# Performance work log

Hardware: AMD Instinct MI355X
Metric: run time of the kernel (lower is better)

The kernel has to match this reference:

```python
import jax, jax.numpy as jnp
import numpy as np

N_ATOMS = 100000
N_EDGES = 3200000
N_RBF = 8
HIDDEN = 16
NUM_GRAPHS = 1


def setup_inputs() -> dict:
    key = jax.random.key(0)
    ks = jax.random.split(key, 10)
    positions = jax.random.normal(ks[0], (N_ATOMS, 3), dtype=jnp.float32)
    vectors = jax.random.normal(ks[1], (N_EDGES, 3), dtype=jnp.float32)
    local_or_ghost = jax.random.uniform(ks[2], (N_ATOMS,), dtype=jnp.float32)
    W1 = jax.random.normal(ks[3], (N_RBF, HIDDEN), dtype=jnp.float32) * 0.1
    b1 = jax.random.normal(ks[4], (HIDDEN,), dtype=jnp.float32) * 0.1
    W2 = jax.random.normal(ks[5], (HIDDEN, HIDDEN), dtype=jnp.float32) * 0.1
    w3 = jax.random.normal(ks[6], (HIDDEN,), dtype=jnp.float32) * 0.1
    field = jax.random.normal(ks[7], (3,), dtype=jnp.float32) * 0.01
    alphas = jax.random.uniform(ks[8], (N_RBF,), dtype=jnp.float32, minval=0.1, maxval=1.1)
    edge_index = jax.random.randint(ks[9], (2, N_EDGES), 0, N_ATOMS, dtype=jnp.int64)
    batch = jnp.zeros((N_ATOMS,), dtype=jnp.int64)
    return {"positions": positions, "vectors": vectors, "local_or_ghost": local_or_ghost,
            "W1": W1, "b1": b1, "W2": W2, "w3": w3, "field": field, "alphas": alphas,
            "edge_index": edge_index, "batch": batch}


def _node_energy(positions, vectors, W1, b1, W2, w3, field, alphas, receiver, n_atoms):
    # Surrogate MACE-like energy: radial basis on edge vectors -> edge MLP ->
    # scatter to receiving atom -> node MLP, plus a linear position term.
    r2 = jnp.sum(vectors * vectors, axis=-1)              # (E,)
    phi = jnp.exp(-r2[:, None] * alphas[None, :])         # (E, F)
    msg = jax.nn.silu(phi @ W1 + b1)                      # (E, H)
    h = jax.ops.segment_sum(msg, receiver, num_segments=n_atoms)  # (N, H)
    node_e = jax.nn.silu(h @ W2) @ w3 + positions @ field          # (N,)
    return node_e


def reference(positions, vectors, local_or_ghost, W1, b1, W2, w3, field, alphas, edge_index, batch):
    n_atoms = positions.shape[0]
    sender, receiver = edge_index[0], edge_index[1]

    def total_local(pos, vec):
        ne = _node_energy(pos, vec, W1, b1, W2, w3, field, alphas, receiver, n_atoms)
        return jnp.sum(ne * local_or_ghost), ne

    # forces = -dE/dpositions, edge_forces = -dE/dvectors (vectors as independent leaf)
    (_, node_energy), grads = jax.value_and_grad(total_local, argnums=(0, 1), has_aux=True)(positions, vectors)
    forces = -grads[0]
    edge_forces = -grads[1]

    node_energy_local = node_energy * local_or_ghost
    total_energy_local = jax.ops.segment_sum(node_energy_local, batch, num_segments=NUM_GRAPHS)

    # edge virial: einsum('zi,zj->zij')
    edge_virial = edge_forces[:, :, None] * vectors[:, None, :]   # (E, 3, 3)
    av_send = jax.ops.segment_sum(edge_virial, sender, num_segments=n_atoms)
    av_recv = jax.ops.segment_sum(edge_virial, receiver, num_segments=n_atoms)
    atom_virial = (av_send + av_recv) * 0.5
    atom_virial = (atom_virial + jnp.swapaxes(atom_virial, -1, -2)) * 0.5
    atom_virial = -atom_virial
    virials = jnp.sum(atom_virial, axis=0)                        # (3, 3)

    return total_energy_local, node_energy, forces, virials, atom_virial
```

## Files before the change

kernel.cpp:

```cpp
#include <hip/hip_runtime.h>

#define N_ATOMS 100000
#define N_EDGES 3200000
#define N_RBF 8
#define HIDDEN 16

#define NB 4096
#define TSCALE 64.0f

#define OFF_TE   0
#define OFF_NE   1
#define OFF_F    (1 + N_ATOMS)
#define OFF_VIR  (1 + N_ATOMS + 3*N_ATOMS)
#define OFF_AV   (OFF_VIR + 9)

#define WPAD (N_ATOMS + 4)
#define NBLK16 (N_ATOMS / 16)
#define SCAN_B 1024
#define SCAN_NB ((N_ATOMS + SCAN_B) / SCAN_B)

#define NTAB_S   0
#define NTAB_G   (NB*HIDDEN)
#define NOFF_R   (2*NB*HIDDEN)
#define NOFF_S   (NOFF_R + WPAD)
#define NCNT_R8  (NOFF_S + WPAD)
#define NCNT_S8  (NCNT_R8 + 8*WPAD)
#define NTEP     (NCNT_S8 + 8*WPAD)
#define NVPART   (NTEP + 8192)
#define NAV6R    (NVPART + 40960)
#define NPAY_R   (NAV6R + 6*N_ATOMS)
#define NDR2V    (NPAY_R + 4*N_EDGES)
#define NBSUM    NPAY_R
#define NEND     (NDR2V + 4*N_EDGES)

#define WOFF_OFFS_R 0
#define WOFF_OFFS_S WPAD
#define WOFF_RANK_R (2*WPAD)
#define WOFF_RANK_S (WOFF_RANK_R + N_EDGES)
#define WOFF_EID_R  (WOFF_RANK_S + N_EDGES)
#define WOFF_EID_S  (WOFF_EID_R + N_EDGES)
#define WOFF_DR2    (WOFF_EID_S + N_EDGES)
#define WOFF_AV6    (WOFF_DR2 + N_EDGES)
#define WOFF_END    (WOFF_AV6 + 6*N_ATOMS)

typedef float fvec4 __attribute__((ext_vector_type(4)));

__device__ inline void nt_store4(float a, float b, float c, float d, float4* p) {
    fvec4 t;
    t.x = a; t.y = b; t.z = c; t.w = d;
    __builtin_nontemporal_store(t, (fvec4*)p);
}

__device__ inline unsigned int get_xcd() {
    unsigned int xcd;
    asm volatile("s_getreg_b32 %0, hwreg(HW_REG_XCC_ID)" : "=s"(xcd));
    return xcd & 7;
}

__global__ void build_tables(const float* __restrict__ W1, const float* __restrict__ b1,
                             const float* __restrict__ alphas,
                             float* __restrict__ s_tab, float* __restrict__ g_tab) {
    int idx = blockIdx.x * blockDim.x + threadIdx.x;
    int b = idx >> 4, j = idx & 15;
    float r2 = (float)b / TSCALE;
    float pre = b1[j], pw = 0.f;
    #pragma unroll
    for (int f = 0; f < N_RBF; ++f) {
        float al = alphas[f];
        float ph = __expf(-r2 * al);
        float w  = W1[f*HIDDEN + j];
        pre += ph * w;
        pw  += al * ph * w;
    }
    float sig = 1.f / (1.f + __expf(-pre));
    s_tab[idx] = pre * sig;
    g_tab[idx] = sig * (1.f + pre * (1.f - sig)) * pw;
}


__global__ void count8_kernel(const int* __restrict__ ei,
                              int* __restrict__ cnt_r8, int* __restrict__ cnt_s8) {
    unsigned int xcd = get_xcd();
    int e = blockIdx.x * blockDim.x + threadIdx.x;
    if (e >= N_EDGES) return;
    int send = ei[e], recv = ei[N_EDGES + e];
    __hip_atomic_fetch_add(&cnt_r8[xcd * WPAD + recv], 1,
                           __ATOMIC_RELAXED, __HIP_MEMORY_SCOPE_WORKGROUP);
    __hip_atomic_fetch_add(&cnt_s8[xcd * WPAD + send], 1,
                           __ATOMIC_RELAXED, __HIP_MEMORY_SCOPE_WORKGROUP);
}

__global__ void xcd_prefix_kernel(int* __restrict__ cnt_r8, int* __restrict__ cnt_s8,
                                  int* __restrict__ offs_r, int* __restrict__ offs_s) {
    int a = blockIdx.x * blockDim.x + threadIdx.x;
    if (a >= N_ATOMS) return;
    int t = 0;
    #pragma unroll
    for (int x = 0; x < 8; ++x) {
        int c = cnt_r8[x*WPAD + a];
        cnt_r8[x*WPAD + a] = t;
        t += c;
    }
    offs_r[a] = t;
    t = 0;
    #pragma unroll
    for (int x = 0; x < 8; ++x) {
        int c = cnt_s8[x*WPAD + a];
        cnt_s8[x*WPAD + a] = t;
        t += c;
    }
    offs_s[a] = t;
}


__global__ void scanA(int* __restrict__ offs_r, int* __restrict__ offs_s,
                      int* __restrict__ bsum) {
    int y = blockIdx.y;
    int* a = y ? offs_s : offs_r;
    const int n = N_ATOMS + 1;
    int i = blockIdx.x * SCAN_B + threadIdx.x;
    int v = (i < n) ? a[i] : 0;
    int lane = threadIdx.x & 63, w = threadIdx.x >> 6;
    int s = v;
    #pragma unroll
    for (int o = 1; o < 64; o <<= 1) {
        int t = __shfl_up(s, o);
        if (lane >= o) s += t;
    }
    __shared__ int wsum[16];
    if (lane == 63) wsum[w] = s;
    __syncthreads();
    if (threadIdx.x < 16) {
        int sc = wsum[threadIdx.x];
        #pragma unroll
        for (int o = 1; o < 16; o <<= 1) {
            int t = __shfl_up(sc, o);
            if ((int)threadIdx.x >= o) sc += t;
        }
        wsum[threadIdx.x] = sc;
    }
    __syncthreads();
    int wpre = (w > 0) ? wsum[w-1] : 0;
    if (i < n) a[i] = s - v + wpre;
    if (threadIdx.x == 0) bsum[y * SCAN_NB + blockIdx.x] = wsum[15];
}

__global__ void scanB(int* __restrict__ bsum) {
    __shared__ int lds[SCAN_NB];
    for (int y = 0; y < 2; ++y) {
        if (threadIdx.x < SCAN_NB) lds[threadIdx.x] = bsum[y*SCAN_NB + threadIdx.x];
        __syncthreads();
        if (threadIdx.x == 0) {
            int run = 0;
            for (int i = 0; i < SCAN_NB; ++i) { int t = lds[i]; lds[i] = run; run += t; }
        }
        __syncthreads();
        if (threadIdx.x < SCAN_NB) bsum[y*SCAN_NB + threadIdx.x] = lds[threadIdx.x];
        __syncthreads();
    }
}

__global__ void scanC(int* __restrict__ offs_r, int* __restrict__ offs_s,
                      const int* __restrict__ bsum) {
    int y = blockIdx.y;
    int* a = y ? offs_s : offs_r;
    int i = blockIdx.x * SCAN_B + threadIdx.x;
    if (i < N_ATOMS + 1) a[i] += bsum[y*SCAN_NB + blockIdx.x];
}

__global__ void scatter1(const int* __restrict__ ei,
                         const int* __restrict__ offs_r, const int* __restrict__ offs_s,
                         int* __restrict__ cnt_r8, int* __restrict__ cnt_s8,
                         const float* __restrict__ vectors,
                         float4* __restrict__ pay_r) {
    unsigned int xcd = get_xcd();
    int e = blockIdx.x * blockDim.x + threadIdx.x;
    if (e >= N_EDGES) return;
    int send = ei[e], recv = ei[N_EDGES + e];
    int br = __hip_atomic_fetch_add(&cnt_r8[xcd*WPAD + recv], 1,
                                    __ATOMIC_RELAXED, __HIP_MEMORY_SCOPE_WORKGROUP);
    int rs = offs_r[recv] + br;
    int bs = __hip_atomic_fetch_add(&cnt_s8[xcd*WPAD + send], 1,
                                    __ATOMIC_RELAXED, __HIP_MEMORY_SCOPE_WORKGROUP);
    int ss = offs_s[send] + bs;
    float vx = vectors[3*e], vy = vectors[3*e+1], vz = vectors[3*e+2];
    nt_store4(vx, vy, vz, __int_as_float(ss), &pay_r[rs]);
}


__global__ void fused16(const float4* __restrict__ pay_r,
                        const float* __restrict__ positions,
                        const float* __restrict__ lg,
                        const float* __restrict__ W2, const float* __restrict__ w3,
                        const float* __restrict__ field,
                        const int* __restrict__ offs_r,
                        const float* __restrict__ s_tab, const float* __restrict__ g_tab,
                        float4* __restrict__ dr2v_s, float* __restrict__ av6r,
                        float* __restrict__ tepart, float* __restrict__ out) {
    int tid = blockIdx.x * blockDim.x + threadIdx.x;
    int a = tid >> 4;
    int sl = threadIdx.x & 15;
    int lane = threadIdx.x & 63;
    int gb = lane & 48;
    int start = offs_r[a], end = offs_r[a + 1];
    int k0 = start + sl;

    float m[HIDDEN];
    #pragma unroll
    for (int j = 0; j < HIDDEN; ++j) m[j] = 0.f;

    for (int k = k0; k < end; k += 16) {
        float4 p = pay_r[k];
        float r2 = p.x*p.x + p.y*p.y + p.z*p.z;
        float x = fminf(r2 * TSCALE, (float)(NB - 2) + 0.999f);
        int i = (int)x;
        float f = x - (float)i;
        const float4* r0 = (const float4*)(s_tab + i * HIDDEN);
        const float4* r1 = (const float4*)(s_tab + (i + 1) * HIDDEN);
        #pragma unroll
        for (int q = 0; q < 4; ++q) {
            float4 A = r0[q], B = r1[q];
            m[4*q+0] += A.x + f * (B.x - A.x);
            m[4*q+1] += A.y + f * (B.y - A.y);
            m[4*q+2] += A.z + f * (B.z - A.z);
            m[4*q+3] += A.w + f * (B.w - A.w);
        }
    }

    #pragma unroll
    for (int o = 1; o < 16; o <<= 1) {
        #pragma unroll
        for (int j = 0; j < HIDDEN; ++j) m[j] += __shfl_xor(m[j], o);
    }

    float aj = 0.f;
    #pragma unroll
    for (int i = 0; i < HIDDEN; ++i) aj += m[i] * W2[i*HIDDEN + sl];
    float sigj = 1.f / (1.f + __expf(-aj));
    float l = lg[a];
    float w3j = w3[sl];
    float sd = aj * sigj * w3j;
    #pragma unroll
    for (int o = 1; o < 16; o <<= 1) sd += __shfl_xor(sd, o);
    float dAj = l * w3j * sigj * (1.f + aj * (1.f - sigj));
    float gown = 0.f;
    #pragma unroll
    for (int q = 0; q < HIDDEN; ++q) {
        float dq = __shfl(dAj, gb | q);
        gown += dq * W2[sl*HIDDEN + q];
    }
    float g[HIDDEN];
    #pragma unroll
    for (int q = 0; q < HIDDEN; ++q) g[q] = __shfl(gown, gb | q);

    float contrib = 0.f;
    if (sl == 0) {
        float ne = sd + positions[3*a]*field[0] + positions[3*a+1]*field[1]
                      + positions[3*a+2]*field[2];
        out[OFF_NE + a] = ne;
        out[OFF_F + 3*a + 0] = -l * field[0];
        out[OFF_F + 3*a + 1] = -l * field[1];
        out[OFF_F + 3*a + 2] = -l * field[2];
        contrib = ne * l;
    }

    float axx=0.f, axy=0.f, axz=0.f, ayy=0.f, ayz=0.f, azz=0.f;
    for (int k = k0; k < end; k += 16) {
        float4 p = pay_r[k];
        float r2 = p.x*p.x + p.y*p.y + p.z*p.z;
        float x = fminf(r2 * TSCALE, (float)(NB - 2) + 0.999f);
        int i = (int)x;
        float f = x - (float)i;
        const float4* r0 = (const float4*)(g_tab + i * HIDDEN);
        const float4* r1 = (const float4*)(g_tab + (i + 1) * HIDDEN);
        float dr2 = 0.f;
        #pragma unroll
        for (int q = 0; q < 4; ++q) {
            float4 A = r0[q], B = r1[q];
            dr2 -= g[4*q+0] * (A.x + f * (B.x - A.x));
            dr2 -= g[4*q+1] * (A.y + f * (B.y - A.y));
            dr2 -= g[4*q+2] * (A.z + f * (B.z - A.z));
            dr2 -= g[4*q+3] * (A.w + f * (B.w - A.w));
        }
        int ss = __float_as_int(p.w);
        nt_store4(p.x, p.y, p.z, dr2, &dr2v_s[ss]);
        axx += dr2*p.x*p.x; axy += dr2*p.x*p.y; axz += dr2*p.x*p.z;
        ayy += dr2*p.y*p.y; ayz += dr2*p.y*p.z; azz += dr2*p.z*p.z;
    }
    #pragma unroll
    for (int o = 1; o < 16; o <<= 1) {
        axx += __shfl_xor(axx, o); axy += __shfl_xor(axy, o); axz += __shfl_xor(axz, o);
        ayy += __shfl_xor(ayy, o); ayz += __shfl_xor(ayz, o); azz += __shfl_xor(azz, o);
    }
    if (sl == 0) {
        float2* p = (float2*)(av6r + (size_t)a * 6);
        p[0] = make_float2(axx, axy);
        p[1] = make_float2(axz, ayy);
        p[2] = make_float2(ayz, azz);
    }

    __shared__ float red[4];
    if (sl != 0) contrib = 0.f;
    contrib += __shfl_xor(contrib, 16);
    contrib += __shfl_xor(contrib, 32);
    int w = threadIdx.x >> 6;
    if (lane == 0) red[w] = contrib;
    __syncthreads();
    if (threadIdx.x == 0) tepart[blockIdx.x] = red[0]+red[1]+red[2]+red[3];
}


__global__ void bwd_send16(const float4* __restrict__ dr2v_s,
                           const int* __restrict__ offs_s,
                           const float* __restrict__ av6r,
                           float* __restrict__ vpart, float* __restrict__ out) {
    int tid = blockIdx.x * blockDim.x + threadIdx.x;
    int a = tid >> 4;
    int sl = threadIdx.x & 15;
    int start = offs_s[a], end = offs_s[a + 1];
    float axx=0.f, axy=0.f, axz=0.f, ayy=0.f, ayz=0.f, azz=0.f;
    for (int k = start + sl; k < end; k += 16) {
        float4 q = dr2v_s[k];
        float dr2 = q.w;
        axx += dr2*q.x*q.x; axy += dr2*q.x*q.y; axz += dr2*q.x*q.z;
        ayy += dr2*q.y*q.y; ayz += dr2*q.y*q.z; azz += dr2*q.z*q.z;
    }
    #pragma unroll
    for (int o = 1; o < 16; o <<= 1) {
        axx += __shfl_xor(axx, o); axy += __shfl_xor(axy, o); axz += __shfl_xor(axz, o);
        ayy += __shfl_xor(ayy, o); ayz += __shfl_xor(ayz, o); azz += __shfl_xor(azz, o);
    }
    __shared__ float sh6[16][6];
    int grp = threadIdx.x >> 4;
    if (sl == 0) {
        const float2* p = (const float2*)(av6r + (size_t)a * 6);
        float2 p0 = p[0], p1 = p[1], p2 = p[2];
        axx += p0.x; axy += p0.y; axz += p1.x;
        ayy += p1.y; ayz += p2.x; azz += p2.y;
        float* o9 = out + OFF_AV + (size_t)a * 9;
        o9[0] = axx; o9[1] = axy; o9[2] = axz;
        o9[3] = axy; o9[4] = ayy; o9[5] = ayz;
        o9[6] = axz; o9[7] = ayz; o9[8] = azz;
        sh6[grp][0] = axx; sh6[grp][1] = axy; sh6[grp][2] = axz;
        sh6[grp][3] = ayy; sh6[grp][4] = ayz; sh6[grp][5] = azz;
    }
    __syncthreads();
    if (threadIdx.x < 6) {
        float s = 0.f;
        #pragma unroll
        for (int q = 0; q < 16; ++q) s += sh6[q][threadIdx.x];
        vpart[blockIdx.x * 6 + threadIdx.x] = s;
    }
}


__global__ void finalize_kernel(const float* __restrict__ tepart,
                                const float* __restrict__ vpart,
                                float* __restrict__ out) {
    int t = threadIdx.x;
    float acc[7];
    #pragma unroll
    for (int c = 0; c < 7; ++c) acc[c] = 0.f;
    for (int i = t; i < NBLK16; i += 1024) {
        acc[0] += tepart[i];
        const float* p = vpart + (size_t)i * 6;
        acc[1] += p[0]; acc[2] += p[1]; acc[3] += p[2];
        acc[4] += p[3]; acc[5] += p[4]; acc[6] += p[5];
    }
    #pragma unroll
    for (int c = 0; c < 7; ++c) {
        #pragma unroll
        for (int o = 1; o < 64; o <<= 1) acc[c] += __shfl_xor(acc[c], o);
    }
    __shared__ float sh[16][8];
    int lane = t & 63, w = t >> 6;
    if (lane == 0) {
        #pragma unroll
        for (int c = 0; c < 7; ++c) sh[w][c] = acc[c];
    }
    __syncthreads();
    if (t == 0) {
        float s[7];
        #pragma unroll
        for (int c = 0; c < 7; ++c) {
            float v = 0.f;
            #pragma unroll
            for (int q = 0; q < 16; ++q) v += sh[q][c];
            s[c] = v;
        }
        out[OFF_TE] = s[0];
        out[OFF_VIR + 0] = s[1]; out[OFF_VIR + 1] = s[2]; out[OFF_VIR + 2] = s[3];
        out[OFF_VIR + 3] = s[2]; out[OFF_VIR + 4] = s[4]; out[OFF_VIR + 5] = s[5];
        out[OFF_VIR + 6] = s[3]; out[OFF_VIR + 7] = s[5]; out[OFF_VIR + 8] = s[6];
    }
}


__global__ void count_kernel(const int* __restrict__ ei,
                             int* __restrict__ cnt_r, int* __restrict__ cnt_s,
                             int* __restrict__ rank_r, int* __restrict__ rank_s) {
    int e = blockIdx.x * blockDim.x + threadIdx.x;
    if (e >= N_EDGES) return;
    int send = ei[e], recv = ei[N_EDGES + e];
    rank_r[e] = atomicAdd(&cnt_r[recv], 1);
    rank_s[e] = atomicAdd(&cnt_s[send], 1);
}

__global__ void scan_kernel(int* __restrict__ offs_r, int* __restrict__ offs_s) {
    int* a = (blockIdx.x == 0) ? offs_r : offs_s;
    const int n = N_ATOMS + 1;
    __shared__ int wsum[4];
    __shared__ int carry_s;
    if (threadIdx.x == 0) carry_s = 0;
    __syncthreads();
    int lane = threadIdx.x & 63, w = threadIdx.x >> 6;
    for (int base = 0; base < n; base += 256) {
        int i = base + threadIdx.x;
        int v = (i < n) ? a[i] : 0;
        int s = v;
        #pragma unroll
        for (int o = 1; o < 64; o <<= 1) {
            int t = __shfl_up(s, o);
            if (lane >= o) s += t;
        }
        if (lane == 63) wsum[w] = s;
        __syncthreads();
        int wpre = 0;
        for (int k = 0; k < w; ++k) wpre += wsum[k];
        int incl = s + wpre;
        int total = wsum[0] + wsum[1] + wsum[2] + wsum[3];
        int excl = incl - v + carry_s;
        if (i < n) a[i] = excl;
        __syncthreads();
        if (threadIdx.x == 0) carry_s += total;
        __syncthreads();
    }
}

__global__ void scatter_kernel(const int* __restrict__ ei,
                               const int* __restrict__ offs_r, const int* __restrict__ offs_s,
                               const int* __restrict__ rank_r, const int* __restrict__ rank_s,
                               int* __restrict__ eid_r, int* __restrict__ eid_s) {
    int e = blockIdx.x * blockDim.x + threadIdx.x;
    if (e >= N_EDGES) return;
    int send = ei[e], recv = ei[N_EDGES + e];
    eid_r[offs_r[recv] + rank_r[e]] = e;
    eid_s[offs_s[send] + rank_s[e]] = e;
}

__global__ void fused_kernel(const float* __restrict__ vectors,
                             const float* __restrict__ positions,
                             const float* __restrict__ lg,
                             const float* __restrict__ W1, const float* __restrict__ b1,
                             const float* __restrict__ W2, const float* __restrict__ w3,
                             const float* __restrict__ field, const float* __restrict__ alphas,
                             const int* __restrict__ offs_r, const int* __restrict__ eid_r,
                             float* __restrict__ dr2buf, float* __restrict__ av6,
                             float* __restrict__ out) {
    int a = (blockIdx.x * blockDim.x + threadIdx.x) >> 6;
    int lane = threadIdx.x & 63;
    int start = offs_r[a], end = offs_r[a + 1];
    float al[N_RBF];
    #pragma unroll
    for (int f = 0; f < N_RBF; ++f) al[f] = alphas[f];
    float m[HIDDEN];
    #pragma unroll
    for (int j = 0; j < HIDDEN; ++j) m[j] = 0.f;
    float t[HIDDEN], paw[HIDDEN];
    float vx0 = 0.f, vy0 = 0.f, vz0 = 0.f;
    int e0 = -1;
    int k0 = start + lane;
    for (int k = k0; k < end; k += 64) {
        int e = eid_r[k];
        float vx = vectors[3*e], vy = vectors[3*e+1], vz = vectors[3*e+2];
        float r2 = vx*vx + vy*vy + vz*vz;
        float phi[N_RBF], apf[N_RBF];
        #pragma unroll
        for (int f = 0; f < N_RBF; ++f) { phi[f] = __expf(-r2 * al[f]); apf[f] = al[f] * phi[f]; }
        bool first = (k == k0);
        if (first) { e0 = e; vx0 = vx; vy0 = vy; vz0 = vz; }
        #pragma unroll
        for (int j = 0; j < HIDDEN; ++j) {
            float pre = b1[j];
            float pw = 0.f;
            #pragma unroll
            for (int f = 0; f < N_RBF; ++f) {
                float w = W1[f*HIDDEN + j];
                pre += phi[f] * w;
                pw  += apf[f] * w;
            }
            float sig = 1.f / (1.f + __expf(-pre));
            m[j] += pre * sig;
            if (first) { t[j] = sig * (1.f + pre * (1.f - sig)); paw[j] = pw; }
        }
    }
    #pragma unroll
    for (int o = 1; o < 64; o <<= 1) {
        #pragma unroll
        for (int j = 0; j < HIDDEN; ++j) m[j] += __shfl_xor(m[j], o);
    }
    int jj = lane & 15;
    int gbase = lane & 48;
    float aj = 0.f;
    #pragma unroll
    for (int i = 0; i < HIDDEN; ++i) aj += m[i] * W2[i*HIDDEN + jj];
    float sigj = 1.f / (1.f + __expf(-aj));
    float l = lg[a];
    float sd = aj * sigj * w3[jj];
    #pragma unroll
    for (int o = 1; o < 16; o <<= 1) sd += __shfl_xor(sd, o);
    float dAj = l * w3[jj] * sigj * (1.f + aj * (1.f - sigj));
    float dAv[HIDDEN];
    #pragma unroll
    for (int q = 0; q < HIDDEN; ++q) dAv[q] = __shfl(dAj, gbase | q);
    float gown = 0.f;
    #pragma unroll
    for (int j2 = 0; j2 < HIDDEN; ++j2) gown += dAv[j2] * W2[jj*HIDDEN + j2];
    float g[HIDDEN];
    #pragma unroll
    for (int q = 0; q < HIDDEN; ++q) g[q] = __shfl(gown, gbase | q);
    float contrib = 0.f;
    if (lane == 0) {
        float ne = sd + positions[3*a]*field[0] + positions[3*a+1]*field[1]
                      + positions[3*a+2]*field[2];
        out[OFF_NE + a] = ne;
        out[OFF_F + 3*a + 0] = -l * field[0];
        out[OFF_F + 3*a + 1] = -l * field[1];
        out[OFF_F + 3*a + 2] = -l * field[2];
        contrib = ne * l;
    }
    float axx=0.f, axy=0.f, axz=0.f, ayy=0.f, ayz=0.f, azz=0.f;
    if (k0 < end) {
        float dr2 = 0.f;
        #pragma unroll
        for (int j = 0; j < HIDDEN; ++j) dr2 -= (g[j] * t[j]) * paw[j];
        dr2buf[e0] = dr2;
        axx = dr2*vx0*vx0; axy = dr2*vx0*vy0; axz = dr2*vx0*vz0;
        ayy = dr2*vy0*vy0; ayz = dr2*vy0*vz0; azz = dr2*vz0*vz0;
    }
    for (int k = k0 + 64; k < end; k += 64) {
        int e = eid_r[k];
        float vx = vectors[3*e], vy = vectors[3*e+1], vz = vectors[3*e+2];
        float r2 = vx*vx + vy*vy + vz*vz;
        float phi[N_RBF], apf[N_RBF];
        #pragma unroll
        for (int f = 0; f < N_RBF; ++f) { phi[f] = __expf(-r2 * al[f]); apf[f] = al[f] * phi[f]; }
        float dr2 = 0.f;
        #pragma unroll
        for (int j = 0; j < HIDDEN; ++j) {
            float pre = b1[j];
            float pw = 0.f;
            #pragma unroll
            for (int f = 0; f < N_RBF; ++f) {
                float w = W1[f*HIDDEN + j];
                pre += phi[f] * w;
                pw  += apf[f] * w;
            }
            float sig = 1.f / (1.f + __expf(-pre));
            float tt = sig * (1.f + pre * (1.f - sig));
            dr2 -= (g[j] * tt) * pw;
        }
        dr2buf[e] = dr2;
        axx += dr2*vx*vx; axy += dr2*vx*vy; axz += dr2*vx*vz;
        ayy += dr2*vy*vy; ayz += dr2*vy*vz; azz += dr2*vz*vz;
    }
    #pragma unroll
    for (int o = 1; o < 64; o <<= 1) {
        axx += __shfl_xor(axx, o); axy += __shfl_xor(axy, o); axz += __shfl_xor(axz, o);
        ayy += __shfl_xor(ayy, o); ayz += __shfl_xor(ayz, o); azz += __shfl_xor(azz, o);
    }
    if (lane == 0) {
        float2* p = (float2*)(av6 + (size_t)a * 6);
        p[0] = make_float2(axx, axy);
        p[1] = make_float2(axz, ayy);
        p[2] = make_float2(ayz, azz);
    }
    __shared__ float red[4];
    int w = threadIdx.x >> 6;
    if (lane == 0) red[w] = contrib;
    __syncthreads();
    if (threadIdx.x == 0) atomicAdd(&out[OFF_TE], red[0]+red[1]+red[2]+red[3]);
}

__global__ void bwd_send_kernel(const float* __restrict__ vectors,
                                const int* __restrict__ offs_s, const int* __restrict__ eid_s,
                                const float* __restrict__ dr2buf, const float* __restrict__ av6,
                                float* __restrict__ out) {
    int a = (blockIdx.x * blockDim.x + threadIdx.x) >> 6;
    int lane = threadIdx.x & 63;
    int start = offs_s[a], end = offs_s[a + 1];
    float axx=0.f, axy=0.f, axz=0.f, ayy=0.f, ayz=0.f, azz=0.f;
    for (int k = start + lane; k < end; k += 64) {
        int e = eid_s[k];
        float dr2 = dr2buf[e];
        float vx = vectors[3*e], vy = vectors[3*e+1], vz = vectors[3*e+2];
        axx += dr2*vx*vx; axy += dr2*vx*vy; axz += dr2*vx*vz;
        ayy += dr2*vy*vy; ayz += dr2*vy*vz; azz += dr2*vz*vz;
    }
    #pragma unroll
    for (int o = 1; o < 64; o <<= 1) {
        axx += __shfl_xor(axx, o); axy += __shfl_xor(axy, o); axz += __shfl_xor(axz, o);
        ayy += __shfl_xor(ayy, o); ayz += __shfl_xor(ayz, o); azz += __shfl_xor(azz, o);
    }
    if (lane == 0) {
        const float2* p = (const float2*)(av6 + (size_t)a * 6);
        float2 p0 = p[0], p1 = p[1], p2 = p[2];
        axx += p0.x; axy += p0.y; axz += p1.x;
        ayy += p1.y; ayz += p2.x; azz += p2.y;
        float* o9 = out + OFF_AV + (size_t)a * 9;
        o9[0] = axx; o9[1] = axy; o9[2] = axz;
        o9[3] = axy; o9[4] = ayy; o9[5] = ayz;
        o9[6] = axz; o9[7] = ayz; o9[8] = azz;
    }
}

__global__ void virial_reduce(float* __restrict__ out) {
    const float* av = out + OFF_AV;
    float acc[9];
    #pragma unroll
    for (int c = 0; c < 9; ++c) acc[c] = 0.0f;
    for (int n = blockIdx.x * blockDim.x + threadIdx.x; n < N_ATOMS;
         n += gridDim.x * blockDim.x) {
        #pragma unroll
        for (int c = 0; c < 9; ++c) acc[c] += av[n*9 + c];
    }
    __shared__ float red[4];
    int lane = threadIdx.x & 63, wid = threadIdx.x >> 6;
    #pragma unroll
    for (int c = 0; c < 9; ++c) {
        float v = acc[c];
        #pragma unroll
        for (int o = 32; o > 0; o >>= 1) v += __shfl_down(v, o);
        if (lane == 0) red[wid] = v;
        __syncthreads();
        if (threadIdx.x == 0) atomicAdd(&out[OFF_VIR + c], red[0]+red[1]+red[2]+red[3]);
        __syncthreads();
    }
}


extern "C" void kernel_launch(void* const* d_in, const int* in_sizes, int n_in,
                              void* d_out, int out_size, void* d_ws, size_t ws_size,
                              hipStream_t stream) {
    const float* positions = (const float*)d_in[0];
    const float* vectors   = (const float*)d_in[1];
    const float* lg        = (const float*)d_in[2];
    const float* W1        = (const float*)d_in[3];
    const float* b1        = (const float*)d_in[4];
    const float* W2        = (const float*)d_in[5];
    const float* w3        = (const float*)d_in[6];
    const float* field     = (const float*)d_in[7];
    const float* alphas    = (const float*)d_in[8];
    const int*   edge_index= (const int*)  d_in[9];
    float* out = (float*)d_out;
    int*   wsi = (int*)d_ws;
    float* wsf = (float*)d_ws;

    dim3 blk(256);
    dim3 egrid((N_EDGES + 255) / 256);
    dim3 g16(NBLK16);

    if (ws_size >= (size_t)NEND * 4) {
        float*  s_tab  = wsf + NTAB_S;
        float*  g_tab  = wsf + NTAB_G;
        int*    offs_r = wsi + NOFF_R;
        int*    offs_s = wsi + NOFF_S;
        int*    cnt_r8 = wsi + NCNT_R8;
        int*    cnt_s8 = wsi + NCNT_S8;
        float*  tepart = wsf + NTEP;
        float*  vpart  = wsf + NVPART;
        float*  av6r   = wsf + NAV6R;
        float4* pay_r  = (float4*)(wsf + NPAY_R);
        float4* dr2v_s = (float4*)(wsf + NDR2V);
        int*    bsum   = wsi + NBSUM;

        hipMemsetAsync(offs_r, 0, (size_t)18 * WPAD * sizeof(int), stream);

        build_tables<<<dim3(NB*HIDDEN/256), blk, 0, stream>>>(W1, b1, alphas, s_tab, g_tab);
        count8_kernel<<<egrid, blk, 0, stream>>>(edge_index, cnt_r8, cnt_s8);
        xcd_prefix_kernel<<<dim3((N_ATOMS+255)/256), blk, 0, stream>>>(cnt_r8, cnt_s8,
                                                                       offs_r, offs_s);
        scanA<<<dim3(SCAN_NB, 2), dim3(SCAN_B), 0, stream>>>(offs_r, offs_s, bsum);
        scanB<<<dim3(1), dim3(256), 0, stream>>>(bsum);
        scanC<<<dim3(SCAN_NB, 2), dim3(SCAN_B), 0, stream>>>(offs_r, offs_s, bsum);
        scatter1<<<egrid, blk, 0, stream>>>(edge_index, offs_r, offs_s,
                                            cnt_r8, cnt_s8, vectors, pay_r);
        fused16<<<g16, blk, 0, stream>>>(pay_r, positions, lg, W2, w3, field,
                                         offs_r, s_tab, g_tab, dr2v_s, av6r, tepart, out);
        bwd_send16<<<g16, blk, 0, stream>>>(dr2v_s, offs_s, av6r, vpart, out);
        finalize_kernel<<<dim3(1), dim3(1024), 0, stream>>>(tepart, vpart, out);
    } else {
        int*   offs_r = wsi + WOFF_OFFS_R;
        int*   offs_s = wsi + WOFF_OFFS_S;
        int*   rank_r = wsi + WOFF_RANK_R;
        int*   rank_s = wsi + WOFF_RANK_S;
        int*   eid_r  = wsi + WOFF_EID_R;
        int*   eid_s  = wsi + WOFF_EID_S;
        float* dr2buf = wsf + WOFF_DR2;
        float* av6    = wsf + WOFF_AV6;
        dim3 agrid(N_ATOMS / 4);

        hipMemsetAsync(offs_r, 0, (size_t)2 * WPAD * sizeof(int), stream);
        hipMemsetAsync(out + OFF_TE, 0, sizeof(float), stream);
        hipMemsetAsync(out + OFF_VIR, 0, 9 * sizeof(float), stream);

        count_kernel<<<egrid, blk, 0, stream>>>(edge_index, offs_r, offs_s, rank_r, rank_s);
        scan_kernel<<<dim3(2), blk, 0, stream>>>(offs_r, offs_s);
        scatter_kernel<<<egrid, blk, 0, stream>>>(edge_index, offs_r, offs_s,
                                                  rank_r, rank_s, eid_r, eid_s);
        fused_kernel<<<agrid, blk, 0, stream>>>(vectors, positions, lg, W1, b1, W2, w3,
                                                field, alphas, offs_r, eid_r, dr2buf, av6, out);
        bwd_send_kernel<<<agrid, blk, 0, stream>>>(vectors, offs_s, eid_s, dr2buf, av6, out);
        virial_reduce<<<dim3(256), blk, 0, stream>>>(out);
    }
}
```

Before: 734.9 us.

## Replace per-atom receiver counting sort with two-pass bucketed radix partition

The receiver-side CSR build changes from per-atom global atomics plus a full prefix scan into a coarse bucket pass (256 atoms per bucket) into a staging buffer, followed by a per-bucket LDS counting sort that also writes offs_r. This cuts global atomic contention and removes one of the two full-length scans. In exchange it adds an extra 16-byte-per-edge staging pass, packs the local receiver id into the upper bits of the sender slot, and reuses the dr2v buffer as the staging area.

```diff
diff --git a/kernel.cpp b/kernel.cpp
--- a/kernel.cpp
+++ b/kernel.cpp
@@ -19,19 +19,27 @@
 #define SCAN_B 1024
 #define SCAN_NB ((N_ATOMS + SCAN_B) / SCAN_B)
 
+#define BSH2   8
+#define BATOMS 256
+#define NBUCK2 391
+#define BPAD2  400
+
 #define NTAB_S   0
 #define NTAB_G   (NB*HIDDEN)
-#define NOFF_R   (2*NB*HIDDEN)
-#define NOFF_S   (NOFF_R + WPAD)
-#define NCNT_R8  (NOFF_S + WPAD)
-#define NCNT_S8  (NCNT_R8 + 8*WPAD)
-#define NTEP     (NCNT_S8 + 8*WPAD)
-#define NVPART   (NTEP + 8192)
-#define NAV6R    (NVPART + 40960)
-#define NPAY_R   (NAV6R + 6*N_ATOMS)
-#define NDR2V    (NPAY_R + 4*N_EDGES)
+#define NBKC8    (2*NB*HIDDEN)
+#define NCNT_S8  (NBKC8 + 8*BPAD2)
+#define NBKO     (NCNT_S8 + 8*WPAD)
+#define NOFF_S   (NBKO + BPAD2)
+#define NOFF_R   (NOFF_S + WPAD)
+#define NTEP     (NOFF_R + WPAD)
+#define NVPART   (NTEP + 6252)
+#define NAV6R    (NVPART + 37504)
+#define NPAY_R_  (NAV6R + 6*N_ATOMS)
+#define NPAY_R   ((NPAY_R_ + 3) & ~3)
+#define NSTG1    (NPAY_R + 4*N_EDGES)
+#define NDR2V    NSTG1
 #define NBSUM    NPAY_R
-#define NEND     (NDR2V + 4*N_EDGES)
+#define NEND     (NSTG1 + 4*N_EDGES)
 
 #define WOFF_OFFS_R 0
 #define WOFF_OFFS_S WPAD
@@ -78,31 +86,43 @@
 }
 
 
-__global__ void count8_kernel(const int* __restrict__ ei,
-                              int* __restrict__ cnt_r8, int* __restrict__ cnt_s8) {
+__global__ void count2(const int* __restrict__ ei,
+                       int* __restrict__ bkc8, int* __restrict__ cnt_s8) {
     unsigned int xcd = get_xcd();
     int e = blockIdx.x * blockDim.x + threadIdx.x;
     if (e >= N_EDGES) return;
     int send = ei[e], recv = ei[N_EDGES + e];
-    __hip_atomic_fetch_add(&cnt_r8[xcd * WPAD + recv], 1,
+    __hip_atomic_fetch_add(&bkc8[xcd*BPAD2 + (recv >> BSH2)], 1,
                            __ATOMIC_RELAXED, __HIP_MEMORY_SCOPE_WORKGROUP);
-    __hip_atomic_fetch_add(&cnt_s8[xcd * WPAD + send], 1,
+    __hip_atomic_fetch_add(&cnt_s8[xcd*WPAD + send], 1,
                            __ATOMIC_RELAXED, __HIP_MEMORY_SCOPE_WORKGROUP);
 }
 
-__global__ void xcd_prefix_kernel(int* __restrict__ cnt_r8, int* __restrict__ cnt_s8,
-                                  int* __restrict__ offs_r, int* __restrict__ offs_s) {
+__global__ void bucket_prefix2(int* __restrict__ bkc8, int* __restrict__ bko) {
+    int tid = threadIdx.x;
+    __shared__ int tot[BPAD2];
+    for (int b = tid; b < NBUCK2; b += 1024) {
+        int t = 0;
+        #pragma unroll
+        for (int x = 0; x < 8; ++x) {
+            int c = bkc8[x*BPAD2 + b];
+            bkc8[x*BPAD2 + b] = t;
+            t += c;
+        }
+        tot[b] = t;
+    }
+    __syncthreads();
+    if (tid == 0) {
+        int run = 0;
+        for (int b = 0; b < NBUCK2; ++b) { bko[b] = run; run += tot[b]; }
+        bko[NBUCK2] = run;
+    }
+}
+
+__global__ void xcd_prefix_s(int* __restrict__ cnt_s8, int* __restrict__ offs_s) {
     int a = blockIdx.x * blockDim.x + threadIdx.x;
     if (a >= N_ATOMS) return;
     int t = 0;
-    #pragma unroll
-    for (int x = 0; x < 8; ++x) {
-        int c = cnt_r8[x*WPAD + a];
-        cnt_r8[x*WPAD + a] = t;
-        t += c;
-    }
-    offs_r[a] = t;
-    t = 0;
     #pragma unroll
     for (int x = 0; x < 8; ++x) {
         int c = cnt_s8[x*WPAD + a];
@@ -113,10 +133,7 @@
 }
 
 
-__global__ void scanA(int* __restrict__ offs_r, int* __restrict__ offs_s,
-                      int* __restrict__ bsum) {
-    int y = blockIdx.y;
-    int* a = y ? offs_s : offs_r;
+__global__ void scanA1(int* __restrict__ a, int* __restrict__ bsum) {
     const int n = N_ATOMS + 1;
     int i = blockIdx.x * SCAN_B + threadIdx.x;
     int v = (i < n) ? a[i] : 0;
@@ -142,49 +159,102 @@
     __syncthreads();
     int wpre = (w > 0) ? wsum[w-1] : 0;
     if (i < n) a[i] = s - v + wpre;
-    if (threadIdx.x == 0) bsum[y * SCAN_NB + blockIdx.x] = wsum[15];
-}
-
-__global__ void scanB(int* __restrict__ bsum) {
+    if (threadIdx.x == 0) bsum[blockIdx.x] = wsum[15];
+}
+
+__global__ void scanB1(int* __restrict__ bsum) {
     __shared__ int lds[SCAN_NB];
-    for (int y = 0; y < 2; ++y) {
-        if (threadIdx.x < SCAN_NB) lds[threadIdx.x] = bsum[y*SCAN_NB + threadIdx.x];
-        __syncthreads();
-        if (threadIdx.x == 0) {
-            int run = 0;
-            for (int i = 0; i < SCAN_NB; ++i) { int t = lds[i]; lds[i] = run; run += t; }
-        }
-        __syncthreads();
-        if (threadIdx.x < SCAN_NB) bsum[y*SCAN_NB + threadIdx.x] = lds[threadIdx.x];
-        __syncthreads();
-    }
-}
-
-__global__ void scanC(int* __restrict__ offs_r, int* __restrict__ offs_s,
-                      const int* __restrict__ bsum) {
-    int y = blockIdx.y;
-    int* a = y ? offs_s : offs_r;
+    if (threadIdx.x < SCAN_NB) lds[threadIdx.x] = bsum[threadIdx.x];
+    __syncthreads();
+    if (threadIdx.x == 0) {
+        int run = 0;
+        for (int i = 0; i < SCAN_NB; ++i) { int t = lds[i]; lds[i] = run; run += t; }
+    }
+    __syncthreads();
+    if (threadIdx.x < SCAN_NB) bsum[threadIdx.x] = lds[threadIdx.x];
+}
+
+__global__ void scanC1(int* __restrict__ a, const int* __restrict__ bsum) {
     int i = blockIdx.x * SCAN_B + threadIdx.x;
-    if (i < N_ATOMS + 1) a[i] += bsum[y*SCAN_NB + blockIdx.x];
-}
-
-__global__ void scatter1(const int* __restrict__ ei,
-                         const int* __restrict__ offs_r, const int* __restrict__ offs_s,
-                         int* __restrict__ cnt_r8, int* __restrict__ cnt_s8,
-                         const float* __restrict__ vectors,
-                         float4* __restrict__ pay_r) {
+    if (i < N_ATOMS + 1) a[i] += bsum[blockIdx.x];
+}
+
+__global__ void part1(const int* __restrict__ ei, const int* __restrict__ bko,
+                      int* __restrict__ bkc8, int* __restrict__ cnt_s8,
+                      const int* __restrict__ offs_s,
+                      const float* __restrict__ vectors,
+                      float4* __restrict__ stg1) {
     unsigned int xcd = get_xcd();
     int e = blockIdx.x * blockDim.x + threadIdx.x;
     if (e >= N_EDGES) return;
     int send = ei[e], recv = ei[N_EDGES + e];
-    int br = __hip_atomic_fetch_add(&cnt_r8[xcd*WPAD + recv], 1,
-                                    __ATOMIC_RELAXED, __HIP_MEMORY_SCOPE_WORKGROUP);
-    int rs = offs_r[recv] + br;
+    int b = recv >> BSH2;
+    int p = __hip_atomic_fetch_add(&bkc8[xcd*BPAD2 + b], 1,
+                                   __ATOMIC_RELAXED, __HIP_MEMORY_SCOPE_WORKGROUP);
+    int ps = bko[b] + p;
     int bs = __hip_atomic_fetch_add(&cnt_s8[xcd*WPAD + send], 1,
                                     __ATOMIC_RELAXED, __HIP_MEMORY_SCOPE_WORKGROUP);
     int ss = offs_s[send] + bs;
     float vx = vectors[3*e], vy = vectors[3*e+1], vz = vectors[3*e+2];
-    nt_store4(vx, vy, vz, __int_as_float(ss), &pay_r[rs]);
+    int packed = ss | ((recv & 255) << 22);
+    stg1[ps] = make_float4(vx, vy, vz, __int_as_float(packed));
+}
+
+
+__global__ __launch_bounds__(1024) void part2(const float4* __restrict__ stg1,
+                                              const int* __restrict__ bko,
+                                              float4* __restrict__ pay_r,
+                                              int* __restrict__ offs_r) {
+    int b = blockIdx.x;
+    int tid = threadIdx.x;
+    int base = bko[b], nE = bko[b+1] - base;
+
+    __shared__ int lcnt[BATOMS];
+    __shared__ int lincl[BATOMS];
+    __shared__ int lalloc[BATOMS];
+    __shared__ int wsum4[4];
+
+    if (tid < BATOMS) lcnt[tid] = 0;
+    __syncthreads();
+
+    for (int k = tid; k < nE; k += 1024) {
+        int pk = __float_as_int(stg1[base + k].w);
+        atomicAdd(&lcnt[((unsigned)pk >> 22) & 255], 1);
+    }
+    __syncthreads();
+
+    if (tid < BATOMS) {
+        int v = lcnt[tid];
+        int lane = tid & 63, w = tid >> 6;
+        int s = v;
+        #pragma unroll
+        for (int o = 1; o < 64; o <<= 1) {
+            int t = __shfl_up(s, o);
+            if (lane >= o) s += t;
+        }
+        lincl[tid] = s;
+        if (lane == 63) wsum4[w] = s;
+    }
+    __syncthreads();
+    if (tid < BATOMS) {
+        int w = tid >> 6;
+        int wpre = 0;
+        for (int k = 0; k < w; ++k) wpre += wsum4[k];
+        int excl = lincl[tid] - lcnt[tid] + wpre;
+        lalloc[tid] = excl;
+        int atom = b * BATOMS + tid;
+        if (atom <= N_ATOMS) offs_r[atom] = base + excl;
+    }
+    __syncthreads();
+
+    for (int k = tid; k < nE; k += 1024) {
+        float4 p = stg1[base + k];
+        int pk = __float_as_int(p.w);
+        int rl = ((unsigned)pk >> 22) & 255;
+        int ss = pk & 0x3FFFFF;
+        int r = atomicAdd(&lalloc[rl], 1);
+        pay_r[base + r] = make_float4(p.x, p.y, p.z, __int_as_float(ss));
+    }
 }
 
 
@@ -353,7 +423,6 @@
     }
 }
 
-
 __global__ void finalize_kernel(const float* __restrict__ tepart,
                                 const float* __restrict__ vpart,
                                 float* __restrict__ out) {
@@ -663,28 +732,32 @@
     if (ws_size >= (size_t)NEND * 4) {
         float*  s_tab  = wsf + NTAB_S;
         float*  g_tab  = wsf + NTAB_G;
+        int*    bkc8   = wsi + NBKC8;
+        int*    cnt_s8 = wsi + NCNT_S8;
+        int*    bko    = wsi + NBKO;
+        int*    offs_s = wsi + NOFF_S;
         int*    offs_r = wsi + NOFF_R;
-        int*    offs_s = wsi + NOFF_S;
-        int*    cnt_r8 = wsi + NCNT_R8;
-        int*    cnt_s8 = wsi + NCNT_S8;
         float*  tepart = wsf + NTEP;
         float*  vpart  = wsf + NVPART;
         float*  av6r   = wsf + NAV6R;
         float4* pay_r  = (float4*)(wsf + NPAY_R);
+        float4* stg1   = (float4*)(wsf + NSTG1);
         float4* dr2v_s = (float4*)(wsf + NDR2V);
         int*    bsum   = wsi + NBSUM;
 
-        hipMemsetAsync(offs_r, 0, (size_t)18 * WPAD * sizeof(int), stream);
+        hipMemsetAsync(bkc8, 0,
+                       (size_t)(8*BPAD2 + 8*WPAD + BPAD2 + WPAD) * sizeof(int), stream);
 
         build_tables<<<dim3(NB*HIDDEN/256), blk, 0, stream>>>(W1, b1, alphas, s_tab, g_tab);
-        count8_kernel<<<egrid, blk, 0, stream>>>(edge_index, cnt_r8, cnt_s8);
-        xcd_prefix_kernel<<<dim3((N_ATOMS+255)/256), blk, 0, stream>>>(cnt_r8, cnt_s8,
-                                                                       offs_r, offs_s);
-        scanA<<<dim3(SCAN_NB, 2), dim3(SCAN_B), 0, stream>>>(offs_r, offs_s, bsum);
-        scanB<<<dim3(1), dim3(256), 0, stream>>>(bsum);
-        scanC<<<dim3(SCAN_NB, 2), dim3(SCAN_B), 0, stream>>>(offs_r, offs_s, bsum);
-        scatter1<<<egrid, blk, 0, stream>>>(edge_index, offs_r, offs_s,
-                                            cnt_r8, cnt_s8, vectors, pay_r);
+        count2<<<egrid, blk, 0, stream>>>(edge_index, bkc8, cnt_s8);
+        bucket_prefix2<<<dim3(1), dim3(1024), 0, stream>>>(bkc8, bko);
+        xcd_prefix_s<<<dim3((N_ATOMS+255)/256), blk, 0, stream>>>(cnt_s8, offs_s);
+        scanA1<<<dim3(SCAN_NB), dim3(SCAN_B), 0, stream>>>(offs_s, bsum);
+        scanB1<<<dim3(1), dim3(128), 0, stream>>>(bsum);
+        scanC1<<<dim3(SCAN_NB), dim3(SCAN_B), 0, stream>>>(offs_s, bsum);
+        part1<<<egrid, blk, 0, stream>>>(edge_index, bko, bkc8, cnt_s8, offs_s,
+                                         vectors, stg1);
+        part2<<<dim3(NBUCK2), dim3(1024), 0, stream>>>(stg1, bko, pay_r, offs_r);
         fused16<<<g16, blk, 0, stream>>>(pay_r, positions, lg, W2, w3, field,
                                          offs_r, s_tab, g_tab, dr2v_s, av6r, tepart, out);
         bwd_send16<<<g16, blk, 0, stream>>>(dr2v_s, offs_s, av6r, vpart, out);
```

After: 766.4 us. +4.3%, slower.
